# Kernel tuning notes

Hardware: AMD Instinct MI355X
Metric: run time of the kernel (lower is better)

The kernel has to match this reference:

```python
import jax, jax.numpy as jnp
import numpy as np

BS, GS, E, KMAX = 128, 2000, 128, 4
CLIP = 10.0
NEG = -1e30


def _gru(x, hprev, Wih, Whh, bih, bhh):
    # torch.nn.GRUCell math
    gi = x @ Wih.T + bih
    gh = hprev @ Whh.T + bhh
    ir, iz, i_n = jnp.split(gi, 3, axis=-1)
    hr, hz, h_n = jnp.split(gh, 3, axis=-1)
    r = jax.nn.sigmoid(ir + hr)
    z = jax.nn.sigmoid(iz + hz)
    n = jnp.tanh(i_n + r * h_n)
    return (1.0 - z) * n + z * hprev


def setup_inputs() -> dict:
    key = jax.random.key(0)
    it = iter(jax.random.split(key, 40))
    s = 1.0 / float(np.sqrt(E))
    u = lambda shape: jax.random.uniform(next(it), shape, jnp.float32, -s, s)
    inp = {
        "h": jax.random.normal(next(it), (BS, GS, E), jnp.float32),
        "rec": jax.random.randint(next(it), (BS, GS), 0, GS, dtype=jnp.int32),
        "context2": jax.random.normal(next(it), (BS, 9), jnp.float32),
        "visited_time": jax.random.randint(next(it), (BS, GS), 0, GS, dtype=jnp.int32),
        "last_action": jax.random.randint(next(it), (BS, 1), 0, GS, dtype=jnp.int32),
        "fixed_action": jax.random.randint(next(it), (BS, KMAX), 0, GS, dtype=jnp.int32),
    }
    for n in ["W_K1", "W_K2", "W_K3", "W_K4", "W_Q1", "W_Q2", "W_Q3", "W_Q4", "W_init"]:
        inp[n] = u((E, E))
    for n in ["b_init", "V1", "V2", "init_query"]:
        inp[n] = u((E,))
    for r in ["rnn1", "rnn2"]:
        inp[r + "_Wih"] = u((3 * E, E))
        inp[r + "_Whh"] = u((3 * E, E))
        inp[r + "_bih"] = u((3 * E,))
        inp[r + "_bhh"] = u((3 * E,))
    return inp


def _forward(h, rec, visited_time, last_action, fixed_action,
             W_K1, W_K2, W_K3, W_K4, W_Q1, W_Q2, W_Q3, W_Q4, V1, V2,
             W_init, b_init, init_query,
             rnn1_Wih, rnn1_Whh, rnn1_bih, rnn1_bhh,
             rnn2_Wih, rnn2_Whh, rnn2_bih, rnn2_bhh):
    bs, gs, e = h.shape
    cols = jnp.arange(gs)[None, :]          # [1, gs]
    rows = jnp.arange(bs)
    # K projections of h are loop-invariant: hoist them (same math as in-loop recompute)
    K1h = jnp.einsum('bge,fe->bgf', h, W_K1)
    K2h = jnp.einsum('bge,fe->bgf', h, W_K2)
    K3h = jnp.einsum('bge,fe->bgf', h, W_K3)
    K4h = jnp.einsum('bge,fe->bgf', h, W_K4)
    q1 = q2 = h.mean(1) @ W_init.T + b_init
    input_q1 = input_q2 = jnp.broadcast_to(init_query, (bs, e))
    mask = jnp.zeros((bs, gs), bool)
    stopped = jnp.ones((bs,), bool)
    nol = jnp.full((bs, 1), -1, jnp.int32)   # next_of_last_action
    ai = jnp.zeros((bs, KMAX), jnp.int32)    # action_index
    kl = jnp.zeros((bs, KMAX + 1), jnp.int32)
    kr = jnp.zeros((bs, KMAX), jnp.int32)
    ll = jnp.zeros((bs,), h.dtype)
    vtt = None
    for i in range(KMAX):
        q1 = _gru(input_q1, q1, rnn1_Wih, rnn1_Whh, rnn1_bih, rnn1_bhh)
        q2 = _gru(input_q2, q2, rnn2_Wih, rnn2_Whh, rnn2_bih, rnn2_bhh)
        s1 = (V1 * jnp.tanh(K1h + (q1 @ W_Q1.T)[:, None, :] + K3h * (q1 @ W_Q3.T)[:, None, :])).sum(-1)
        s2 = (V2 * jnp.tanh(K2h + (q2 @ W_Q2.T)[:, None, :] + K4h * (q2 @ W_Q4.T)[:, None, :])).sum(-1)
        logits = jnp.tanh(s1 + s2) * CLIP
        logits = jnp.where(mask, NEG, logits)
        if i == 0:
            logits = jnp.where(cols == last_action, NEG, logits)
        action = fixed_action[:, i:i + 1]
        if i > 0:
            action = jnp.where(stopped[:, None], ai[:, 0:1], action)
        logp = jax.nn.log_softmax(logits, axis=-1)
        loss_now = jnp.take_along_axis(logp, action, 1)[:, 0]
        ll = ll + (loss_now if i == 0 else jnp.where(stopped, 0.0, loss_now))
        nna = jnp.take_along_axis(rec, action, 1)  # next_of_new_action [bs,1]
        ai = ai.at[:, i].set(action[:, 0])
        kl = kl.at[:, i].set(jnp.where(stopped, action[:, 0], kl[:, i]))
        kr = kr.at[:, (i - 1) % KMAX].set(jnp.where(stopped, kr[:, (i - 1) % KMAX], action[:, 0]))
        kl = kl.at[:, i + 1].set(nna[:, 0])
        input_q1 = h[rows, action[:, 0]]
        input_q2 = jnp.where(stopped[:, None], input_q1, h[rows, nol[:, 0] % gs])
        eq = (action == nol)[:, 0]
        stopped = eq if i == 0 else (stopped | eq)
        kl = kl.at[:, i].set(jnp.where(stopped, kl[:, (i - 1) % (KMAX + 1)], kl[:, i]))
        kr = kr.at[:, i].set(jnp.where(stopped, kr[:, (i - 1) % KMAX], kr[:, i]))
        if i == 0:
            vtt = (visited_time - jnp.take_along_axis(visited_time, action, 1)) % gs
        vtt_a = jnp.take_along_axis(vtt, action, 1)
        mask = vtt <= vtt_a
        if i == 0:
            mask = mask | (vtt > gs - 2)
        mask = jnp.where(stopped[:, None] & (cols == action), False, mask)
        allow = (~stopped) & (nna[:, 0] == ai[:, 0])
        mask = jnp.where(allow[:, None] & (cols == ai[:, 0:1]), False, mask)
        nol = jnp.where(stopped[:, None], jnp.int32(-1), nna)
    kr = kr.at[:, KMAX - 1].set(jnp.where(~stopped, kl[:, KMAX], kr[:, KMAX - 1]))
    action_all = jnp.concatenate([ai, kl[:, :KMAX], kr], axis=-1)  # [bs, 3*KMAX]
    return action_all, ll


def reference(h, rec, context2, visited_time, last_action, fixed_action,
              W_K1, W_K2, W_K3, W_K4, W_Q1, W_Q2, W_Q3, W_Q4,
              V1, V2, W_init, b_init, init_query,
              rnn1_Wih, rnn1_Whh, rnn1_bih, rnn1_bhh,
              rnn2_Wih, rnn2_Whh, rnn2_bih, rnn2_bhh):
    # context2 unused: with_explore_stat_feature=False path (learned V1/V2)
    return _forward(h, rec, visited_time, last_action, fixed_action,
                    W_K1, W_K2, W_K3, W_K4, W_Q1, W_Q2, W_Q3, W_Q4, V1, V2,
                    W_init, b_init, init_query,
                    rnn1_Wih, rnn1_Whh, rnn1_bih, rnn1_bhh,
                    rnn2_Wih, rnn2_Whh, rnn2_bih, rnn2_bhh)
```

## Files before the change

### kernel.cpp

```cpp
#include <hip/hip_runtime.h>
#include <math.h>

#define BS 128
#define GS 2000
#define E  128
#define KMAXI 4
#define CLIPV 10.0f
#define NEGV  -1.0e30f

typedef __bf16 bf16_t;
typedef __bf16 bf16x8 __attribute__((ext_vector_type(8)));
typedef __bf16 bf16x4 __attribute__((ext_vector_type(4)));
typedef float fx4 __attribute__((ext_vector_type(4)));

__device__ __forceinline__ float fast_sigmoid(float x){ return 1.0f/(1.0f+__expf(-x)); }
__device__ __forceinline__ float fast_tanhf(float x){
    float e = __expf(2.0f*x);
    return 1.0f - 2.0f/(e + 1.0f);
}
__device__ __forceinline__ float pade_tanh(float x){
    float t = fminf(3.0f, fmaxf(-3.0f, x));
    float r = t*t;
    float num = t*(27.0f + r);
    float den = fmaf(9.0f, r, 27.0f);
    return num * __builtin_amdgcn_rcpf(den);
}
__device__ __forceinline__ int pymod(int a){ int d = a % GS; return d < 0 ? d + GS : d; }

#define SC_STRIDE 64

__global__ __launch_bounds__(128) void k_traj(
    const int* __restrict__ rec, const int* __restrict__ vtime,
    const int* __restrict__ last_action, const int* __restrict__ fixed_action,
    int* __restrict__ sc, float* __restrict__ out)
{
    int b = threadIdx.x;
    if (b >= BS) return;
    int stopped = 1, nol = -1;
    int ai[4]={0,0,0,0}, kl[5]={0,0,0,0,0}, kr[4]={0,0,0,0};
    int a0 = 0;
    int* scb = sc + b*SC_STRIDE;
    for (int it=0; it<KMAXI; ++it){
        int action = (it==0) ? fixed_action[b*KMAXI]
                             : (stopped ? ai[0] : fixed_action[b*KMAXI+it]);
        int old_stopped = stopped;
        if (it==0) a0 = action;
        int vta = (it==0) ? 0 : pymod(vtime[(size_t)b*GS+action] - vtime[(size_t)b*GS+a0]);
        int nna = rec[(size_t)b*GS+action];
        int eq  = (action == nol) ? 1 : 0;
        int new_stopped = (it==0) ? eq : (stopped | eq);
        int ai0 = (it==0) ? action : ai[0];
        int allow = (!new_stopped) && (nna == ai0);

        ai[it] = action;
        if (old_stopped)  kl[it] = action;
        if (!old_stopped) kr[(it+3)&3] = action;
        kl[it+1] = nna;
        if (new_stopped) kl[it] = kl[(it+4)%5];
        if (new_stopped) kr[it] = kr[(it+3)&3];

        int row1 = action;
        int i2 = pymod(nol);
        int row2 = old_stopped ? row1 : i2;

        int* s_it = scb + 8 + it*8;
        s_it[0]=action; s_it[1]=old_stopped; s_it[2]=new_stopped;
        s_it[3]=allow;  s_it[4]=vta; s_it[5]=row1; s_it[6]=row2;

        nol = new_stopped ? -1 : nna;
        stopped = new_stopped;
    }
    scb[0] = a0;
    if (!stopped) kr[3] = kl[4];
    for (int j=0;j<4;++j) out[b*12+j]   = (float)ai[j];
    for (int j=0;j<4;++j) out[b*12+4+j] = (float)kl[j];
    for (int j=0;j<4;++j) out[b*12+8+j] = (float)kr[j];
}

__global__ __launch_bounds__(256) void k_hmean(const float* __restrict__ h, float* __restrict__ hpart){
    int b = blockIdx.x, p = blockIdx.y, tid = threadIdx.x;
    int e4 = (tid & 31) * 4;
    int gsub = tid >> 5;
    float4 acc = {0.f,0.f,0.f,0.f};
    int g0 = p*125, g1 = g0+125;
    for (int g = g0 + gsub; g < g1; g += 8){
        float4 v = *(const float4*)(h + ((size_t)b*GS + g)*E + e4);
        acc.x += v.x; acc.y += v.y; acc.z += v.z; acc.w += v.w;
    }
    __shared__ float ps[8][E];
    *(float4*)(&ps[gsub][e4]) = acc;
    __syncthreads();
    if (tid < E){
        float s = 0.f;
        #pragma unroll
        for (int j=0;j<8;++j) s += ps[j][tid];
        hpart[(b*16+p)*E + tid] = s;
    }
}

__device__ __forceinline__ float dot32(const float* a, const float* __restrict__ w){
    const float4* a4=(const float4*)a; const float4* w4=(const float4*)w;
    float s=0.f;
    #pragma unroll 8
    for (int i=0;i<32;++i){ float4 x=a4[i], y=w4[i]; s += x.x*y.x + x.y*y.y + x.z*y.z + x.w*y.w; }
    return s;
}

__global__ __launch_bounds__(128) void k_gru4(
    const float* __restrict__ hpart, const float* __restrict__ W_init,
    const float* __restrict__ b_init, const float* __restrict__ init_query,
    const float* __restrict__ h, const int* __restrict__ sc,
    const float* __restrict__ Wih1, const float* __restrict__ Whh1,
    const float* __restrict__ bih1, const float* __restrict__ bhh1,
    const float* __restrict__ Wih2, const float* __restrict__ Whh2,
    const float* __restrict__ bih2, const float* __restrict__ bhh2,
    const float* __restrict__ WQ1, const float* __restrict__ WQ2,
    const float* __restrict__ WQ3, const float* __restrict__ WQ4,
    float* __restrict__ add_buf, float* __restrict__ mul_buf)
{
    int b = blockIdx.x, rnn = blockIdx.y, t = threadIdx.x;
    const float* Wih = rnn ? Wih2 : Wih1;
    const float* Whh = rnn ? Whh2 : Whh1;
    const float* bih = rnn ? bih2 : bih1;
    const float* bhh = rnn ? bhh2 : bhh1;
    const float* WQa = rnn ? WQ2 : WQ1;
    const float* WQm = rnn ? WQ4 : WQ3;

    __shared__ float xv[E], hv[E];
    {
        float s = 0.f;
        for (int p=0;p<16;++p) s += hpart[(b*16+p)*E + t];
        xv[t] = s * (1.0f/(float)GS);
    }
    __syncthreads();
    float q0 = b_init[t] + dot32(xv, W_init + (size_t)t*E);
    __syncthreads();
    hv[t] = q0;
    xv[t] = init_query[t];
    __syncthreads();

    for (int s=0; s<KMAXI; ++s){
        if (s>0){
            int row = sc[b*SC_STRIDE + 8 + (s-1)*8 + (rnn==0 ? 5 : 6)];
            xv[t] = h[((size_t)b*GS + row)*E + t];
            __syncthreads();
        }
        float gr=bih[t], gz=bih[t+E], gn=bih[t+2*E];
        float hr=bhh[t], hz=bhh[t+E], hn=bhh[t+2*E];
        {
            const float4* x4 = (const float4*)xv;
            const float4* h4 = (const float4*)hv;
            const float4* wr=(const float4*)(Wih+(size_t)t*E);
            const float4* wz=(const float4*)(Wih+(size_t)(t+E)*E);
            const float4* wn=(const float4*)(Wih+(size_t)(t+2*E)*E);
            const float4* vr=(const float4*)(Whh+(size_t)t*E);
            const float4* vz=(const float4*)(Whh+(size_t)(t+E)*E);
            const float4* vn=(const float4*)(Whh+(size_t)(t+2*E)*E);
            #pragma unroll 4
            for (int i=0;i<32;++i){
                float4 x=x4[i], h0=h4[i];
                float4 a=wr[i];  gr += x.x*a.x + x.y*a.y + x.z*a.z + x.w*a.w;
                float4 bq=wz[i]; gz += x.x*bq.x + x.y*bq.y + x.z*bq.z + x.w*bq.w;
                float4 cq=wn[i]; gn += x.x*cq.x + x.y*cq.y + x.z*cq.z + x.w*cq.w;
                float4 d=vr[i];  hr += h0.x*d.x + h0.y*d.y + h0.z*d.z + h0.w*d.w;
                float4 e=vz[i];  hz += h0.x*e.x + h0.y*e.y + h0.z*e.z + h0.w*e.w;
                float4 f=vn[i];  hn += h0.x*f.x + h0.y*f.y + h0.z*f.z + h0.w*f.w;
            }
        }
        float r = fast_sigmoid(gr+hr);
        float z = fast_sigmoid(gz+hz);
        float n = fast_tanhf(gn + r*hn);
        float hnew = (1.f-z)*n + z*hv[t];
        __syncthreads();
        hv[t] = hnew;
        __syncthreads();
        float a = dot32(hv, WQa + (size_t)t*E);
        float m = dot32(hv, WQm + (size_t)t*E);
        int slot = s*2 + rnn;
        add_buf[(size_t)slot*BS*E + b*E + t] = a;
        mul_buf[(size_t)slot*BS*E + b*E + t] = m;
        __syncthreads();
    }
}

__global__ __launch_bounds__(256) void k_mbuild(
    const float* __restrict__ WK1, const float* __restrict__ WK2,
    const float* __restrict__ WK3, const float* __restrict__ WK4,
    const float* __restrict__ mul_buf, bf16_t* __restrict__ Mb)
{
    int b = blockIdx.x, slot = blockIdx.y, tid = threadIdx.x;
    int arm = slot & 1;
    const float* WKa = arm ? WK2 : WK1;
    const float* WKm = arm ? WK4 : WK3;
    const float* mul = mul_buf + (size_t)slot*BS*E + b*E;
    __shared__ float mv[E];
    if (tid < E) mv[tid] = mul[tid];
    __syncthreads();
    bf16_t* outp = Mb + ((size_t)slot*BS + b)*E*E;
    #pragma unroll 4
    for (int j=0;j<16;++j){
        int u = j*256 + tid;
        int f = u >> 5, e4 = (u & 31) * 4;
        float mf = mv[f];
        float4 a = *(const float4*)(WKa + (size_t)f*E + e4);
        float4 m = *(const float4*)(WKm + (size_t)f*E + e4);
        bf16x4 o;
        o[0]=(bf16_t)(a.x + m.x*mf);
        o[1]=(bf16_t)(a.y + m.y*mf);
        o[2]=(bf16_t)(a.z + m.z*mf);
        o[3]=(bf16_t)(a.w + m.w*mf);
        *(bf16x4*)(outp + (size_t)f*E + e4) = o;
    }
}

__global__ __launch_bounds__(256,2) void k_scores(
    const float* __restrict__ hf, const bf16_t* __restrict__ Mb,
    const float* __restrict__ add_buf,
    const float* __restrict__ V1, const float* __restrict__ V2,
    float* __restrict__ raw4)
{
    constexpr int LDW = 136;
    __shared__ bf16_t sM[E*LDW];
    int b = blockIdx.x, yc = blockIdx.y, tid = threadIdx.x;
    int wave = tid >> 6, lane = tid & 63;
    int qd = lane >> 4, cl = lane & 15;
    int gbase = yc*128 + wave*32;

    bf16x8 afr[2][4];
    #pragma unroll
    for (int set=0; set<2; ++set){
        int grow = gbase + set*16 + cl;
        if (grow >= GS) grow = GS-1;
        const float* hrow = hf + ((size_t)b*GS + grow)*E;
        #pragma unroll
        for (int s=0;s<4;++s){
            const float* p = hrow + s*32 + qd*8;
            float4 u0 = *(const float4*)(p);
            float4 u1 = *(const float4*)(p+4);
            bf16x8 a;
            a[0]=(bf16_t)u0.x; a[1]=(bf16_t)u0.y; a[2]=(bf16_t)u0.z; a[3]=(bf16_t)u0.w;
            a[4]=(bf16_t)u1.x; a[5]=(bf16_t)u1.y; a[6]=(bf16_t)u1.z; a[7]=(bf16_t)u1.w;
            afr[set][s]=a;
        }
    }

    for (int it=0; it<KMAXI; ++it){
        float sp[2][4] = {{0.f,0.f,0.f,0.f},{0.f,0.f,0.f,0.f}};
        #pragma unroll
        for (int arm=0; arm<2; ++arm){
            int slot = it*2 + arm;
            const bf16x8* Gm = (const bf16x8*)(Mb + ((size_t)slot*BS + b)*E*E);
            const float* addv = add_buf + (size_t)slot*BS*E + b*E;
            const float* Vv = arm ? V2 : V1;

            __syncthreads();
            #pragma unroll
            for (int k=0;k<8;++k){
                int u = k*256 + tid;
                bf16x8 v = Gm[u];
                *(bf16x8*)(sM + (u>>4)*LDW + (u&15)*8) = v;
            }
            __syncthreads();

            #pragma unroll
            for (int tf=0; tf<8; ++tf){
                int f = tf*16 + cl;
                bf16x8 b1[4];
                #pragma unroll
                for (int s=0;s<4;++s)
                    b1[s] = *(const bf16x8*)(sM + f*LDW + s*32 + qd*8);
                fx4 a0 = {0.f,0.f,0.f,0.f};
                fx4 a1 = {0.f,0.f,0.f,0.f};
                #pragma unroll
                for (int s=0;s<4;++s){
                    a0 = __builtin_amdgcn_mfma_f32_16x16x32_bf16(afr[0][s], b1[s], a0, 0,0,0);
                    a1 = __builtin_amdgcn_mfma_f32_16x16x32_bf16(afr[1][s], b1[s], a1, 0,0,0);
                }
                float av = addv[f], vv = Vv[f];
                #pragma unroll
                for (int r=0;r<4;++r){
                    sp[0][r] += vv*pade_tanh(a0[r]+av);
                    sp[1][r] += vv*pade_tanh(a1[r]+av);
                }
            }
        }
        #pragma unroll
        for (int set=0;set<2;++set){
            float v[4];
            #pragma unroll
            for (int r=0;r<4;++r){
                float s = sp[set][r];
                s += __shfl_xor(s, 1); s += __shfl_xor(s, 2);
                s += __shfl_xor(s, 4); s += __shfl_xor(s, 8);
                v[r] = s;
            }
            if (cl==0){
                int gi = gbase + set*16 + qd*4;
                if (gi+3 < GS){
                    float4 o;
                    o.x = CLIPV*pade_tanh(v[0]);
                    o.y = CLIPV*pade_tanh(v[1]);
                    o.z = CLIPV*pade_tanh(v[2]);
                    o.w = CLIPV*pade_tanh(v[3]);
                    *(float4*)(raw4 + ((size_t)it*BS + b)*GS + gi) = o;
                }
            }
        }
    }
}

__global__ __launch_bounds__(256) void k_ll(
    const float* __restrict__ raw4, const int* __restrict__ sc,
    const int* __restrict__ vtime, const int* __restrict__ last_action,
    float* __restrict__ out)
{
    __shared__ float sL[GS];
    __shared__ float red[256];
    int b = blockIdx.x, t = threadIdx.x;
    const int* scb = sc + b*SC_STRIDE;
    int a0 = scb[0];
    int la = last_action[b];
    int vt0 = vtime[(size_t)b*GS + a0];
    float ll = 0.f;

    for (int it=0; it<KMAXI; ++it){
        const int* s_it = scb + 8 + it*8;
        int action = s_it[0], olds = s_it[1];
        int ap=0, nsp=0, alp=0, vtp=0, p = it-1;
        if (it>0){
            const int* s_p = scb + 8 + p*8;
            ap = s_p[0]; nsp = s_p[2]; alp = s_p[3]; vtp = s_p[4];
        }
        for (int g=t; g<GS; g+=256){
            float l = raw4[((size_t)it*BS + b)*GS + g];
            int m;
            if (it==0){
                m = (g==la);
            } else {
                int d = pymod(vtime[(size_t)b*GS+g] - vt0);
                m = (d <= vtp) ? 1 : 0;
                if (p==0 && d > GS-2) m = 1;
                if (nsp && g==ap)     m = 0;
                if (alp && g==a0)     m = 0;
            }
            sL[g] = m ? NEGV : l;
        }
        __syncthreads();
        float mx = -3.0e38f;
        for (int g=t; g<GS; g+=256) mx = fmaxf(mx, sL[g]);
        red[t]=mx; __syncthreads();
        for (int s=128;s>0;s>>=1){ if(t<s) red[t]=fmaxf(red[t],red[t+s]); __syncthreads(); }
        mx = red[0]; __syncthreads();
        float sm = 0.f;
        for (int g=t; g<GS; g+=256) sm += __expf(sL[g]-mx);
        red[t]=sm; __syncthreads();
        for (int s=128;s>0;s>>=1){ if(t<s) red[t]+=red[t+s]; __syncthreads(); }
        float lse = mx + __logf(red[0]);
        float loss = sL[action] - lse;
        if (it>0 && olds) loss = 0.f;
        ll += loss;
        __syncthreads();
    }
    if (t==0) out[BS*12 + b] = ll;
}

extern "C" void kernel_launch(void* const* d_in, const int* in_sizes, int n_in,
                              void* d_out, int out_size, void* d_ws, size_t ws_size,
                              hipStream_t stream)
{
    const float* h            = (const float*)d_in[0];
    const int*   rec          = (const int*)  d_in[1];
    const int*   vtime        = (const int*)  d_in[3];
    const int*   last_action  = (const int*)  d_in[4];
    const int*   fixed_action = (const int*)  d_in[5];
    const float* WK1=(const float*)d_in[6],  *WK2=(const float*)d_in[7];
    const float* WK3=(const float*)d_in[8],  *WK4=(const float*)d_in[9];
    const float* WQ1=(const float*)d_in[10], *WQ2=(const float*)d_in[11];
    const float* WQ3=(const float*)d_in[12], *WQ4=(const float*)d_in[13];
    const float* W_init=(const float*)d_in[14];
    const float* b_init=(const float*)d_in[15];
    const float* V1=(const float*)d_in[16], *V2=(const float*)d_in[17];
    const float* init_query=(const float*)d_in[18];
    const float* Wih1=(const float*)d_in[19], *Whh1=(const float*)d_in[20];
    const float* bih1=(const float*)d_in[21], *bhh1=(const float*)d_in[22];
    const float* Wih2=(const float*)d_in[23], *Whh2=(const float*)d_in[24];
    const float* bih2=(const float*)d_in[25], *bhh2=(const float*)d_in[26];
    float* out = (float*)d_out;

    char* ws = (char*)d_ws;
    size_t off = 0;
    auto alloc = [&](size_t bytes)->char*{
        char* p = ws + off; off += (bytes + 255) & ~(size_t)255; return p;
    };
    bf16_t* Mb     = (bf16_t*)alloc((size_t)8*BS*E*E*sizeof(bf16_t));
    float*  raw4   = (float*) alloc((size_t)KMAXI*BS*GS*sizeof(float));
    float*  add_buf= (float*) alloc((size_t)8*BS*E*sizeof(float));
    float*  mul_buf= (float*) alloc((size_t)8*BS*E*sizeof(float));
    float*  hpart  = (float*) alloc((size_t)BS*16*E*sizeof(float));
    int*    sc     = (int*)   alloc((size_t)BS*SC_STRIDE*sizeof(int));
    (void)in_sizes; (void)n_in; (void)out_size; (void)ws_size;

    hipLaunchKernelGGL(k_traj, dim3(1), dim3(128), 0, stream,
                       rec, vtime, last_action, fixed_action, sc, out);
    hipLaunchKernelGGL(k_hmean, dim3(BS,16), dim3(256), 0, stream, h, hpart);
    hipLaunchKernelGGL(k_gru4, dim3(BS,2), dim3(128), 0, stream,
                       hpart, W_init, b_init, init_query, h, sc,
                       Wih1,Whh1,bih1,bhh1, Wih2,Whh2,bih2,bhh2,
                       WQ1,WQ2,WQ3,WQ4, add_buf, mul_buf);
    hipLaunchKernelGGL(k_mbuild, dim3(BS,8), dim3(256), 0, stream,
                       WK1,WK2,WK3,WK4, mul_buf, Mb);
    hipLaunchKernelGGL(k_scores, dim3(BS,16), dim3(256), 0, stream,
                       h, Mb, add_buf, V1, V2, raw4);
    hipLaunchKernelGGL(k_ll, dim3(BS), dim3(256), 0, stream,
                       raw4, sc, vtime, last_action, out);
}
```

Before: 509.3 us.

## Pack tanh into a paired polynomial, seed MFMA with bias, parallelize ll over iterations

```diff
diff --git a/kernel.cpp b/kernel.cpp
--- a/kernel.cpp
+++ b/kernel.cpp
@@ -12,6 +12,7 @@
 typedef __bf16 bf16x8 __attribute__((ext_vector_type(8)));
 typedef __bf16 bf16x4 __attribute__((ext_vector_type(4)));
 typedef float fx4 __attribute__((ext_vector_type(4)));
+typedef float fx2 __attribute__((ext_vector_type(2)));
 
 __device__ __forceinline__ float fast_sigmoid(float x){ return 1.0f/(1.0f+__expf(-x)); }
 __device__ __forceinline__ float fast_tanhf(float x){
@@ -19,11 +20,21 @@
     return 1.0f - 2.0f/(e + 1.0f);
 }
 __device__ __forceinline__ float pade_tanh(float x){
-    float t = fminf(3.0f, fmaxf(-3.0f, x));
+    float t = __builtin_amdgcn_fmed3f(x, -3.0f, 3.0f);
     float r = t*t;
     float num = t*(27.0f + r);
     float den = fmaf(9.0f, r, 27.0f);
     return num * __builtin_amdgcn_rcpf(den);
+}
+__device__ __forceinline__ fx2 tanh2_poly(fx2 x){
+    fx2 t;
+    t.x = __builtin_amdgcn_fmed3f(x.x, -3.0f, 3.0f);
+    t.y = __builtin_amdgcn_fmed3f(x.y, -3.0f, 3.0f);
+    fx2 r = t*t;
+    fx2 q = r*(-0.0015650f) + 0.03172875f;
+    q = q*r + (-0.23082094f);
+    q = q*r + 0.979947f;
+    return t*q;
 }
 __device__ __forceinline__ int pymod(int a){ int d = a % GS; return d < 0 ? d + GS : d; }
 
@@ -72,6 +83,7 @@
     }
     scb[0] = a0;
     if (!stopped) kr[3] = kl[4];
+    out[BS*12 + b] = 0.0f;
     for (int j=0;j<4;++j) out[b*12+j]   = (float)ai[j];
     for (int j=0;j<4;++j) out[b*12+4+j] = (float)kl[j];
     for (int j=0;j<4;++j) out[b*12+8+j] = (float)kr[j];
@@ -213,7 +225,7 @@
     }
 }
 
-__global__ __launch_bounds__(256,2) void k_scores(
+__global__ __launch_bounds__(256,4) void k_scores(
     const float* __restrict__ hf, const bf16_t* __restrict__ Mb,
     const float* __restrict__ add_buf,
     const float* __restrict__ V1, const float* __restrict__ V2,
@@ -245,7 +257,7 @@
     }
 
     for (int it=0; it<KMAXI; ++it){
-        float sp[2][4] = {{0.f,0.f,0.f,0.f},{0.f,0.f,0.f,0.f}};
+        fx2 s00={0.f,0.f}, s01={0.f,0.f}, s10={0.f,0.f}, s11={0.f,0.f};
         #pragma unroll
         for (int arm=0; arm<2; ++arm){
             int slot = it*2 + arm;
@@ -265,31 +277,33 @@
             #pragma unroll
             for (int tf=0; tf<8; ++tf){
                 int f = tf*16 + cl;
+                float av = addv[f], vv = Vv[f];
                 bf16x8 b1[4];
                 #pragma unroll
                 for (int s=0;s<4;++s)
                     b1[s] = *(const bf16x8*)(sM + f*LDW + s*32 + qd*8);
-                fx4 a0 = {0.f,0.f,0.f,0.f};
-                fx4 a1 = {0.f,0.f,0.f,0.f};
+                fx4 a0 = {av,av,av,av};
+                fx4 a1 = {av,av,av,av};
                 #pragma unroll
                 for (int s=0;s<4;++s){
                     a0 = __builtin_amdgcn_mfma_f32_16x16x32_bf16(afr[0][s], b1[s], a0, 0,0,0);
                     a1 = __builtin_amdgcn_mfma_f32_16x16x32_bf16(afr[1][s], b1[s], a1, 0,0,0);
                 }
-                float av = addv[f], vv = Vv[f];
-                #pragma unroll
-                for (int r=0;r<4;++r){
-                    sp[0][r] += vv*pade_tanh(a0[r]+av);
-                    sp[1][r] += vv*pade_tanh(a1[r]+av);
-                }
+                fx2 vv2 = {vv, vv};
+                s00 += vv2 * tanh2_poly((fx2){a0[0], a0[1]});
+                s01 += vv2 * tanh2_poly((fx2){a0[2], a0[3]});
+                s10 += vv2 * tanh2_poly((fx2){a1[0], a1[1]});
+                s11 += vv2 * tanh2_poly((fx2){a1[2], a1[3]});
             }
         }
         #pragma unroll
         for (int set=0;set<2;++set){
-            float v[4];
+            fx2 pa = set ? s10 : s00;
+            fx2 pb = set ? s11 : s01;
+            float v[4] = {pa.x, pa.y, pb.x, pb.y};
             #pragma unroll
             for (int r=0;r<4;++r){
-                float s = sp[set][r];
+                float s = v[r];
                 s += __shfl_xor(s, 1); s += __shfl_xor(s, 2);
                 s += __shfl_xor(s, 4); s += __shfl_xor(s, 8);
                 v[r] = s;
@@ -316,52 +330,47 @@
 {
     __shared__ float sL[GS];
     __shared__ float red[256];
-    int b = blockIdx.x, t = threadIdx.x;
+    int b = blockIdx.x, it = blockIdx.y, t = threadIdx.x;
     const int* scb = sc + b*SC_STRIDE;
+    const int* s_it = scb + 8 + it*8;
+    int action = s_it[0], olds = s_it[1];
+    if (it>0 && olds) return;
     int a0 = scb[0];
     int la = last_action[b];
     int vt0 = vtime[(size_t)b*GS + a0];
-    float ll = 0.f;
-
-    for (int it=0; it<KMAXI; ++it){
-        const int* s_it = scb + 8 + it*8;
-        int action = s_it[0], olds = s_it[1];
-        int ap=0, nsp=0, alp=0, vtp=0, p = it-1;
-        if (it>0){
-            const int* s_p = scb + 8 + p*8;
-            ap = s_p[0]; nsp = s_p[2]; alp = s_p[3]; vtp = s_p[4];
-        }
-        for (int g=t; g<GS; g+=256){
-            float l = raw4[((size_t)it*BS + b)*GS + g];
-            int m;
-            if (it==0){
-                m = (g==la);
-            } else {
-                int d = pymod(vtime[(size_t)b*GS+g] - vt0);
-                m = (d <= vtp) ? 1 : 0;
-                if (p==0 && d > GS-2) m = 1;
-                if (nsp && g==ap)     m = 0;
-                if (alp && g==a0)     m = 0;
-            }
-            sL[g] = m ? NEGV : l;
-        }
-        __syncthreads();
-        float mx = -3.0e38f;
-        for (int g=t; g<GS; g+=256) mx = fmaxf(mx, sL[g]);
-        red[t]=mx; __syncthreads();
-        for (int s=128;s>0;s>>=1){ if(t<s) red[t]=fmaxf(red[t],red[t+s]); __syncthreads(); }
-        mx = red[0]; __syncthreads();
-        float sm = 0.f;
-        for (int g=t; g<GS; g+=256) sm += __expf(sL[g]-mx);
-        red[t]=sm; __syncthreads();
-        for (int s=128;s>0;s>>=1){ if(t<s) red[t]+=red[t+s]; __syncthreads(); }
+    int ap=0, nsp=0, alp=0, vtp=0, p = it-1;
+    if (it>0){
+        const int* s_p = scb + 8 + p*8;
+        ap = s_p[0]; nsp = s_p[2]; alp = s_p[3]; vtp = s_p[4];
+    }
+    for (int g=t; g<GS; g+=256){
+        float l = raw4[((size_t)it*BS + b)*GS + g];
+        int m;
+        if (it==0){
+            m = (g==la);
+        } else {
+            int d = pymod(vtime[(size_t)b*GS+g] - vt0);
+            m = (d <= vtp) ? 1 : 0;
+            if (p==0 && d > GS-2) m = 1;
+            if (nsp && g==ap)     m = 0;
+            if (alp && g==a0)     m = 0;
+        }
+        sL[g] = m ? NEGV : l;
+    }
+    __syncthreads();
+    float mx = -3.0e38f;
+    for (int g=t; g<GS; g+=256) mx = fmaxf(mx, sL[g]);
+    red[t]=mx; __syncthreads();
+    for (int s=128;s>0;s>>=1){ if(t<s) red[t]=fmaxf(red[t],red[t+s]); __syncthreads(); }
+    mx = red[0]; __syncthreads();
+    float sm = 0.f;
+    for (int g=t; g<GS; g+=256) sm += __expf(sL[g]-mx);
+    red[t]=sm; __syncthreads();
+    for (int s=128;s>0;s>>=1){ if(t<s) red[t]+=red[t+s]; __syncthreads(); }
+    if (t==0){
         float lse = mx + __logf(red[0]);
-        float loss = sL[action] - lse;
-        if (it>0 && olds) loss = 0.f;
-        ll += loss;
-        __syncthreads();
-    }
-    if (t==0) out[BS*12 + b] = ll;
+        atomicAdd(&out[BS*12 + b], sL[action] - lse);
+    }
 }
 
 extern "C" void kernel_launch(void* const* d_in, const int* in_sizes, int n_in,
@@ -411,6 +420,6 @@
                        WK1,WK2,WK3,WK4, mul_buf, Mb);
     hipLaunchKernelGGL(k_scores, dim3(BS,16), dim3(256), 0, stream,
                        h, Mb, add_buf, V1, V2, raw4);
-    hipLaunchKernelGGL(k_ll, dim3(BS), dim3(256), 0, stream,
+    hipLaunchKernelGGL(k_ll, dim3(BS, KMAXI), dim3(256), 0, stream,
                        raw4, sc, vtime, last_action, out);
 }
```

Measured after the change: 540.8 us. 1.06x slower.
